# Optimization experiments

Measured on AMD Instinct MI355X. Metric: run time of the kernel, lower is better.

The kernel has to match this reference:

```python
import jax, jax.numpy as jnp
import numpy as np

CW = 64            # channel_width; N = CW**2 = 4096 tokens = d_batch
BIAS = 1.0         # same_channel_bias
D_KQ = 2048
D_V = 2048
STEP = 0           # self.step at first call
T_IDX = 0          # self.t at first call
PE_N = 10000.0


def pe_row(t, d, n=PE_N):
    """Row t of the sinusoidal positional encoding P[t, :] of width d (d even)."""
    i = jnp.arange(d // 2, dtype=jnp.float32)
    denom = jnp.power(jnp.float32(n), 2.0 * i / d)
    ang = jnp.float32(t) / denom
    row = jnp.zeros((d,), dtype=jnp.float32)
    row = row.at[0::2].set(jnp.sin(ang)).at[1::2].set(jnp.cos(ang))
    return row


def setup_inputs() -> dict:
    key = jax.random.key(0)
    ks = jax.random.split(key, 6)
    N = CW * CW          # 4096
    d_in = 2048
    num_steps = 8
    return {
        "x": jax.random.normal(ks[0], (N, d_in), dtype=jnp.float32),
        "W_query": jax.random.uniform(ks[1], (d_in, D_KQ), dtype=jnp.float32),
        "W_key": jax.random.uniform(ks[2], (d_in, D_KQ), dtype=jnp.float32),
        "W_value": jax.random.uniform(ks[3], (d_in, D_V), dtype=jnp.float32),
        "b_channel": jax.random.uniform(ks[4], (N, D_V), dtype=jnp.float32),
        "b_t": jax.random.uniform(ks[5], (num_steps, N, D_V), dtype=jnp.float32),
    }


def reference(x, W_query, W_key, W_value, b_channel, b_t):
    N = x.shape[0]
    q = x @ W_query                      # [N, d_kq]
    k = x @ W_key                        # [N, d_kq]
    v = x @ W_value                      # [N, d_v]
    scores = q @ k.T                     # [N, N]
    # kron(eye(cw), ones(cw,cw)*bias): +bias where tokens share a channel block
    ch = jnp.arange(N) // CW
    scores = scores + jnp.where(ch[:, None] == ch[None, :], jnp.float32(BIAS), jnp.float32(0.0))
    # NOTE: bias added BEFORE the 1/sqrt(d_kq) scaling, as in the original
    attn = jax.nn.softmax(scores / jnp.float32(D_KQ) ** 0.5, axis=-1)
    ctx = attn @ v                       # [N, d_v]
    ctx = ctx + b_channel + b_t[STEP] + pe_row(T_IDX, D_V)
    return ctx
```

## Files before the change

kernel.cpp:

```cpp
#include <hip/hip_runtime.h>
#include <cstdint>
#include <cstddef>


using h8    = __attribute__((ext_vector_type(8))) _Float16;
using h4    = __attribute__((ext_vector_type(4))) _Float16;
using f32x4 = __attribute__((ext_vector_type(4))) float;

__device__ __forceinline__ void gll16(const void* g, void* l) {
  __builtin_amdgcn_global_load_lds(
      (const __attribute__((address_space(1))) uint32_t*)g,
      (__attribute__((address_space(3))) uint32_t*)l, 16, 0, 0);
}

__global__ __launch_bounds__(256) void split_x_kernel(
    const float* __restrict__ X, _Float16* __restrict__ hi,
    _Float16* __restrict__ lo, int n4)
{
  int i = blockIdx.x * 256 + threadIdx.x;
  if (i >= n4) return;
  float4 v = ((const float4*)X)[i];
  float a[4] = {v.x, v.y, v.z, v.w};
  h4 hh, ll;
#pragma unroll
  for (int e = 0; e < 4; ++e) {
    _Float16 h = (_Float16)a[e];
    hh[e] = h;
    ll[e] = (_Float16)(a[e] - (float)h);
  }
  ((h4*)hi)[i] = hh;
  ((h4*)lo)[i] = ll;
}

__global__ __launch_bounds__(256) void transpose_split_w(
    const float* __restrict__ W, _Float16* __restrict__ Thi,
    _Float16* __restrict__ Tlo, int D, int writeLo)
{
  __shared__ float t[32][33];
  int n0 = blockIdx.x * 32;
  int k0 = blockIdx.y * 32;
  int tx = threadIdx.x & 31;
  int ty = threadIdx.x >> 5;
  for (int j = ty; j < 32; j += 8)
    t[j][tx] = W[(size_t)(k0 + j) * D + n0 + tx];
  __syncthreads();
  for (int j = ty; j < 32; j += 8) {
    float v = t[tx][j];
    size_t o = (size_t)(n0 + j) * D + k0 + tx;
    _Float16 h = (_Float16)v;
    Thi[o] = h;
    if (writeLo) Tlo[o] = (_Float16)(v - (float)h);
  }
}

constexpr int EPI_QK = 0;
constexpr int EPI_VT = 1;
constexpr int EPI_S  = 2;
constexpr int EPI_CTX = 3;

template<int EPI, bool SPLIT>
__global__ __launch_bounds__(256, 2) void gemm_bt(
    const _Float16* __restrict__ A, const _Float16* __restrict__ Al,
    const _Float16* __restrict__ B, const _Float16* __restrict__ Bl,
    int K, int lda, int ldb, int ldc, int ldt,
    float* __restrict__ of32, _Float16* __restrict__ oh1,
    _Float16* __restrict__ oh2,
    const float* __restrict__ c1, const float* __restrict__ c2)
{
  __shared__ __align__(16) _Float16 sA [128 * 32];
  __shared__ __align__(16) _Float16 sB [128 * 32];
  __shared__ __align__(16) _Float16 sAl[SPLIT ? 128 * 32 : 8];
  __shared__ __align__(16) _Float16 sBl[SPLIT ? 128 * 32 : 8];

  const int tid  = threadIdx.x;
  const int lane = tid & 63;
  const int wave = tid >> 6;
  const int wm = wave >> 1, wn = wave & 1;
  const int m0 = blockIdx.y * 128, n0 = blockIdx.x * 128;

  const int ca = lane + 64 * wave;
  const int ra = ca >> 2, ka = (ca & 3) * 8;
  const int cc = ca + 256;
  const int rb = cc >> 2, kb = (cc & 3) * 8;
  const size_t lo0 = (size_t)wave * 1024;
  const size_t lo1 = lo0 + 4096;

  const _Float16* gA0 = A + (size_t)(m0 + ra) * lda + ka;
  const _Float16* gA1 = A + (size_t)(m0 + rb) * lda + kb;
  const _Float16* gB0 = B + (size_t)(n0 + ra) * ldb + ka;
  const _Float16* gB1 = B + (size_t)(n0 + rb) * ldb + kb;
  const _Float16* gAl0 = Al ? Al + (size_t)(m0 + ra) * lda + ka : nullptr;
  const _Float16* gAl1 = Al ? Al + (size_t)(m0 + rb) * lda + kb : nullptr;
  const _Float16* gBl0 = Bl ? Bl + (size_t)(n0 + ra) * ldb + ka : nullptr;
  const _Float16* gBl1 = Bl ? Bl + (size_t)(n0 + rb) * ldb + kb : nullptr;

  f32x4 acc[4][4];
#pragma unroll
  for (int i = 0; i < 4; ++i)
#pragma unroll
    for (int j = 0; j < 4; ++j) acc[i][j] = (f32x4){0.f, 0.f, 0.f, 0.f};

  const int fr = lane & 15;
  const int fk = (lane >> 4) * 8;

  for (int k0 = 0; k0 < K; k0 += 32) {
    gll16(gA0 + k0, (char*)sA + lo0);
    gll16(gA1 + k0, (char*)sA + lo1);
    gll16(gB0 + k0, (char*)sB + lo0);
    gll16(gB1 + k0, (char*)sB + lo1);
    if constexpr (SPLIT) {
      gll16(gAl0 + k0, (char*)sAl + lo0);
      gll16(gAl1 + k0, (char*)sAl + lo1);
      gll16(gBl0 + k0, (char*)sBl + lo0);
      gll16(gBl1 + k0, (char*)sBl + lo1);
    }
    __syncthreads();

    h8 af[4], bf[4], afl[4], bfl[4];
#pragma unroll
    for (int mi = 0; mi < 4; ++mi)
      af[mi] = *(const h8*)&sA[(wm * 64 + mi * 16 + fr) * 32 + fk];
#pragma unroll
    for (int ni = 0; ni < 4; ++ni)
      bf[ni] = *(const h8*)&sB[(wn * 64 + ni * 16 + fr) * 32 + fk];
    if constexpr (SPLIT) {
#pragma unroll
      for (int mi = 0; mi < 4; ++mi)
        afl[mi] = *(const h8*)&sAl[(wm * 64 + mi * 16 + fr) * 32 + fk];
#pragma unroll
      for (int ni = 0; ni < 4; ++ni)
        bfl[ni] = *(const h8*)&sBl[(wn * 64 + ni * 16 + fr) * 32 + fk];
    }

#pragma unroll
    for (int mi = 0; mi < 4; ++mi)
#pragma unroll
      for (int ni = 0; ni < 4; ++ni) {
        acc[mi][ni] = __builtin_amdgcn_mfma_f32_16x16x32_f16(
            af[mi], bf[ni], acc[mi][ni], 0, 0, 0);
        if constexpr (SPLIT) {
          acc[mi][ni] = __builtin_amdgcn_mfma_f32_16x16x32_f16(
              af[mi], bfl[ni], acc[mi][ni], 0, 0, 0);
          acc[mi][ni] = __builtin_amdgcn_mfma_f32_16x16x32_f16(
              afl[mi], bf[ni], acc[mi][ni], 0, 0, 0);
        }
      }
    __syncthreads();
  }

  const int drow = (lane >> 4) * 4;
  const int dcol = lane & 15;
#pragma unroll
  for (int mi = 0; mi < 4; ++mi) {
#pragma unroll
    for (int ni = 0; ni < 4; ++ni) {
      const int row = m0 + wm * 64 + mi * 16 + drow;
      const int col = n0 + wn * 64 + ni * 16 + dcol;
      f32x4 v = acc[mi][ni];
      if constexpr (EPI == EPI_S) {
#pragma unroll
        for (int r = 0; r < 4; ++r)
          of32[(size_t)(row + r) * ldc + col] = v[r];
      } else if constexpr (EPI == EPI_QK) {
#pragma unroll
        for (int r = 0; r < 4; ++r) {
          float x = v[r];
          _Float16 hh = (_Float16)x;
          size_t o = (size_t)(row + r) * ldc + col;
          oh1[o] = hh;
          oh2[o] = (_Float16)(x - (float)hh);
        }
      } else if constexpr (EPI == EPI_VT) {
        h4 hh;
#pragma unroll
        for (int r = 0; r < 4; ++r) hh[r] = (_Float16)v[r];
        *(h4*)&oh1[(size_t)col * ldt + row] = hh;
      } else {
#pragma unroll
        for (int r = 0; r < 4; ++r) {
          size_t o = (size_t)(row + r) * ldc + col;
          of32[o] = v[r] + c1[o] + c2[o] + ((col & 1) ? 1.0f : 0.0f);
        }
      }
    }
  }
}

template<int EPI, int NPASS>
__global__ __launch_bounds__(512, 2) void gemm256(
    const _Float16* __restrict__ A0, const _Float16* __restrict__ B0,
    const _Float16* __restrict__ A1, const _Float16* __restrict__ B1,
    const _Float16* __restrict__ A2, const _Float16* __restrict__ B2,
    int lda, int ldb, int ldc,
    float* __restrict__ of32, _Float16* __restrict__ oh1,
    _Float16* __restrict__ oh2)
{
  __shared__ __align__(16) char lds[147456];
  constexpr int T = NPASS * 32;

  const int tid  = threadIdx.x;
  const int lane = tid & 63;
  const int w    = tid >> 6;
  const int wm = w >> 2, wn = w & 3;
  const int fr = lane & 15, sl = lane >> 4;
  const int m0 = blockIdx.y * 256, n0 = blockIdx.x * 256;

  const int sswz  = ((sl ^ ((fr >> 1) & 3)) << 4);
  const int aBase = (wm * 128 + fr) * 64 + sswz;
  const int bBase = 65536 + (wn * 64 + fr) * 64 + sswz;
  const int rowoff = w * 16 + (lane >> 2);
  const int sL8 = ((lane & 3) ^ ((lane >> 3) & 3)) * 8;

  auto gstage = [&](int t, int isB, int kk) {
    const _Float16* g; int ld, r0, gk; char* dst;
    if (t >= T) {
      g = A0; ld = lda; r0 = m0; gk = 0; dst = lds + 131072;
    } else {
      const int p = t >> 5, kt = t & 31;
      g  = isB ? (p == 0 ? B0 : (p == 1 ? B1 : B2))
               : (p == 0 ? A0 : (p == 1 ? A1 : A2));
      ld = isB ? ldb : lda;
      r0 = isB ? n0 : m0;
      gk = kt * 64 + kk * 32;
      dst = lds + (isB ? 65536 : 0) + (t & 1) * 32768 + kk * 16384;
    }
#pragma unroll
    for (int i = 0; i < 2; ++i)
      gll16(g + (size_t)(r0 + i * 128 + rowoff) * ld + gk + sL8,
            dst + i * 8192 + w * 1024);
  };

  f32x4 acc[8][4];
#pragma unroll
  for (int i = 0; i < 8; ++i)
#pragma unroll
    for (int j = 0; j < 4; ++j) acc[i][j] = (f32x4){0.f, 0.f, 0.f, 0.f};

  gstage(0, 0, 0); gstage(0, 1, 0);
  gstage(0, 0, 1); gstage(0, 1, 1);
  gstage(1, 0, 0); gstage(1, 1, 0);
  asm volatile("s_waitcnt vmcnt(8)" ::: "memory");
  __builtin_amdgcn_s_barrier();

#pragma unroll 2
  for (int t = 0; t < T; ++t) {
    const char* aB = lds + (t & 1) * 32768;

#pragma unroll
    for (int kk = 0; kk < 2; ++kk) {
      if (kk == 0) { gstage(t + 1, 0, 1); gstage(t + 1, 1, 1); }
      else         { gstage(t + 2, 0, 0); gstage(t + 2, 1, 0); }

      const char* base = aB + kk * 16384;
      h8 af[8], bf[4];
#pragma unroll
      for (int i = 0; i < 8; ++i)
        af[i] = *(const h8*)(base + aBase + i * 1024);
#pragma unroll
      for (int i = 0; i < 4; ++i)
        bf[i] = *(const h8*)(base + bBase + i * 1024);

      __builtin_amdgcn_s_setprio(1);
#pragma unroll
      for (int mi = 0; mi < 8; ++mi)
#pragma unroll
        for (int ni = 0; ni < 4; ++ni)
          acc[mi][ni] = __builtin_amdgcn_mfma_f32_16x16x32_f16(
              af[mi], bf[ni], acc[mi][ni], 0, 0, 0);
      __builtin_amdgcn_s_setprio(0);

      asm volatile("s_waitcnt vmcnt(8)" ::: "memory");
      __builtin_amdgcn_s_barrier();
    }
  }
  asm volatile("s_waitcnt vmcnt(0)" ::: "memory");

  const int drow = sl * 4;
#pragma unroll
  for (int mi = 0; mi < 8; ++mi) {
#pragma unroll
    for (int ni = 0; ni < 4; ++ni) {
      const int row = m0 + wm * 128 + mi * 16 + drow;
      const int col = n0 + wn * 64 + ni * 16 + fr;
      f32x4 v = acc[mi][ni];
      if constexpr (EPI == EPI_S) {
#pragma unroll
        for (int r = 0; r < 4; ++r)
          of32[(size_t)(row + r) * ldc + col] = v[r];
      } else {
#pragma unroll
        for (int r = 0; r < 4; ++r) {
          float x = v[r];
          _Float16 hh = (_Float16)x;
          size_t o = (size_t)(row + r) * ldc + col;
          oh1[o] = hh;
          oh2[o] = (_Float16)(x - (float)hh);
        }
      }
    }
  }
}

__global__ __launch_bounds__(256) void softmax_bias_kernel(
    float* __restrict__ S, int N)
{
  const float scale = 0.022097086912079608f;
  const int row = blockIdx.x;
  float* rp = S + (size_t)row * N;
  const int cblk = row & ~63;
  const int tid = threadIdx.x;

  float vals[16];
  float mx = -3.0e38f;
#pragma unroll
  for (int it = 0; it < 4; ++it) {
    int base = (it * 256 + tid) * 4;
    float4 v = *(const float4*)(rp + base);
    float a[4] = {v.x, v.y, v.z, v.w};
#pragma unroll
    for (int e = 0; e < 4; ++e) {
      int col = base + e;
      float s = a[e];
      if ((col & ~63) == cblk) s += 1.0f;
      s *= scale;
      vals[it * 4 + e] = s;
      mx = fmaxf(mx, s);
    }
  }
  __shared__ float red[8];
#pragma unroll
  for (int m = 32; m; m >>= 1) mx = fmaxf(mx, __shfl_xor(mx, m, 64));
  if ((tid & 63) == 0) red[tid >> 6] = mx;
  __syncthreads();
  mx = fmaxf(fmaxf(red[0], red[1]), fmaxf(red[2], red[3]));

  float sum = 0.f;
#pragma unroll
  for (int i = 0; i < 16; ++i) {
    float e = __expf(vals[i] - mx);
    vals[i] = e;
    sum += e;
  }
#pragma unroll
  for (int m = 32; m; m >>= 1) sum += __shfl_xor(sum, m, 64);
  if ((tid & 63) == 0) red[4 + (tid >> 6)] = sum;
  __syncthreads();
  sum = red[4] + red[5] + red[6] + red[7];
  float inv = 1.0f / sum;

  _Float16* op = (_Float16*)rp;
#pragma unroll
  for (int it = 0; it < 4; ++it) {
    int base = (it * 256 + tid) * 4;
    h4 hh;
#pragma unroll
    for (int e = 0; e < 4; ++e) hh[e] = (_Float16)(vals[it * 4 + e] * inv);
    *(h4*)(op + base) = hh;
  }
}

extern "C" void kernel_launch(void* const* d_in, const int* in_sizes, int n_in,
                              void* d_out, int out_size, void* d_ws,
                              size_t ws_size, hipStream_t stream)
{
  (void)in_sizes; (void)n_in; (void)out_size; (void)ws_size;
  const float* x   = (const float*)d_in[0];
  const float* Wq  = (const float*)d_in[1];
  const float* Wk  = (const float*)d_in[2];
  const float* Wv  = (const float*)d_in[3];
  const float* bch = (const float*)d_in[4];
  const float* bt0 = (const float*)d_in[5];
  float* out = (float*)d_out;

  char* ws = (char*)d_ws;
  const size_t O_XHI  = 0;
  const size_t O_XLO  = O_XHI + 16777216;
  const size_t O_WQKH = O_XLO + 16777216;
  const size_t O_WQKL = O_WQKH + 16777216;
  const size_t O_S    = 0;
  const size_t O_WVH  = 67108864;
  const size_t O_VT   = O_WVH + 8388608;
  const size_t O_QKH  = O_VT + 16777216;
  const size_t O_QKL  = O_QKH + 33554432;

  _Float16* xhi  = (_Float16*)(ws + O_XHI);
  _Float16* xlo  = (_Float16*)(ws + O_XLO);
  _Float16* wqkh = (_Float16*)(ws + O_WQKH);
  _Float16* wqkl = (_Float16*)(ws + O_WQKL);
  _Float16* wvh  = (_Float16*)(ws + O_WVH);
  _Float16* vT   = (_Float16*)(ws + O_VT);
  _Float16* qkh  = (_Float16*)(ws + O_QKH);
  _Float16* qkl  = (_Float16*)(ws + O_QKL);
  float*    S    = (float*)(ws + O_S);

  split_x_kernel<<<2097152 / 256, 256, 0, stream>>>(x, xhi, xlo, 2097152);
  dim3 tg(64, 64);
  transpose_split_w<<<tg, 256, 0, stream>>>(Wq, wqkh, wqkl, 2048, 1);
  transpose_split_w<<<tg, 256, 0, stream>>>(
      Wk, wqkh + (size_t)2048 * 2048, wqkl + (size_t)2048 * 2048, 2048, 1);
  transpose_split_w<<<tg, 256, 0, stream>>>(Wv, wvh, nullptr, 2048, 0);

  gemm256<EPI_QK, 3><<<dim3(16, 16), 512, 0, stream>>>(
      xhi, wqkh, xhi, wqkl, xlo, wqkh, 2048, 2048, 4096,
      nullptr, qkh, qkl);
  gemm_bt<EPI_VT, false><<<dim3(16, 32), 256, 0, stream>>>(
      xhi, nullptr, wvh, nullptr, 2048, 2048, 2048, 0, 4096,
      nullptr, vT, nullptr, nullptr, nullptr);

  gemm256<EPI_S, 3><<<dim3(16, 16), 512, 0, stream>>>(
      qkh, qkh + 2048, qkh, qkl + 2048, qkl, qkh + 2048, 4096, 4096, 4096,
      S, nullptr, nullptr);

  softmax_bias_kernel<<<4096, 256, 0, stream>>>(S, 4096);

  gemm_bt<EPI_CTX, false><<<dim3(16, 32), 256, 0, stream>>>(
      (const _Float16*)S, nullptr, vT, nullptr, 4096, 8192, 4096, 2048, 0,
      out, nullptr, nullptr, bch, bt0);
}
```

Before: 932.5 us.

## Use triple-buffered LDS ring with register double-buffered fragments in GEMM

Restructures the main GEMM loop from a 2-slot, split-k staging scheme into a 3-slot ring of 32-wide k substeps, with A and B fragments double-buffered in registers. The next substep's LDS reads are issued before the current MFMA block so LDS latency overlaps matrix math, and LDS use drops. In exchange it doubles fragment registers, which could pressure the 2-waves-per-SIMD launch bound. It also relies on a single barrier per substep to guard ring-slot reuse.

```diff
diff --git a/kernel.cpp b/kernel.cpp
--- a/kernel.cpp
+++ b/kernel.cpp
@@ -195,8 +195,8 @@
     float* __restrict__ of32, _Float16* __restrict__ oh1,
     _Float16* __restrict__ oh2)
 {
-  __shared__ __align__(16) char lds[147456];
-  constexpr int T = NPASS * 32;
+  __shared__ __align__(16) char lds[114688];
+  constexpr int S = NPASS * 64;
 
   const int tid  = threadIdx.x;
   const int lane = tid & 63;
@@ -207,27 +207,31 @@
 
   const int sswz  = ((sl ^ ((fr >> 1) & 3)) << 4);
   const int aBase = (wm * 128 + fr) * 64 + sswz;
-  const int bBase = 65536 + (wn * 64 + fr) * 64 + sswz;
+  const int bBase = 16384 + (wn * 64 + fr) * 64 + sswz;
   const int rowoff = w * 16 + (lane >> 2);
   const int sL8 = ((lane & 3) ^ ((lane >> 3) & 3)) * 8;
 
-  auto gstage = [&](int t, int isB, int kk) {
-    const _Float16* g; int ld, r0, gk; char* dst;
-    if (t >= T) {
-      g = A0; ld = lda; r0 = m0; gk = 0; dst = lds + 131072;
+  auto gstage = [&](int u) {
+    const _Float16 *gA, *gB; int gk; char *dstA, *dstB;
+    if (u >= S) {
+      gA = A0; gB = B0; gk = 0;
+      dstA = lds + 98304; dstB = lds + 98304;
     } else {
-      const int p = t >> 5, kt = t & 31;
-      g  = isB ? (p == 0 ? B0 : (p == 1 ? B1 : B2))
-               : (p == 0 ? A0 : (p == 1 ? A1 : A2));
-      ld = isB ? ldb : lda;
-      r0 = isB ? n0 : m0;
-      gk = kt * 64 + kk * 32;
-      dst = lds + (isB ? 65536 : 0) + (t & 1) * 32768 + kk * 16384;
+      const int p = u >> 6, ku = u & 63;
+      gA = (p == 0 ? A0 : (p == 1 ? A1 : A2));
+      gB = (p == 0 ? B0 : (p == 1 ? B1 : B2));
+      gk = ku * 32;
+      char* base = lds + (u % 3) * 32768;
+      dstA = base; dstB = base + 16384;
     }
 #pragma unroll
     for (int i = 0; i < 2; ++i)
-      gll16(g + (size_t)(r0 + i * 128 + rowoff) * ld + gk + sL8,
-            dst + i * 8192 + w * 1024);
+      gll16(gA + (size_t)(m0 + i * 128 + rowoff) * lda + gk + sL8,
+            dstA + i * 8192 + w * 1024);
+#pragma unroll
+    for (int i = 0; i < 2; ++i)
+      gll16(gB + (size_t)(n0 + i * 128 + rowoff) * ldb + gk + sL8,
+            dstB + i * 8192 + w * 1024);
   };
 
   f32x4 acc[8][4];
@@ -236,42 +240,55 @@
 #pragma unroll
     for (int j = 0; j < 4; ++j) acc[i][j] = (f32x4){0.f, 0.f, 0.f, 0.f};
 
-  gstage(0, 0, 0); gstage(0, 1, 0);
-  gstage(0, 0, 1); gstage(0, 1, 1);
-  gstage(1, 0, 0); gstage(1, 1, 0);
-  asm volatile("s_waitcnt vmcnt(8)" ::: "memory");
+  h8 af0[8], bf0[4], af1[8], bf1[4];
+
+  auto ldset0 = [&](int u) {
+    const char* ub = lds + (u % 3) * 32768;
+#pragma unroll
+    for (int i = 0; i < 8; ++i) af0[i] = *(const h8*)(ub + aBase + i * 1024);
+#pragma unroll
+    for (int i = 0; i < 4; ++i) bf0[i] = *(const h8*)(ub + bBase + i * 1024);
+  };
+  auto ldset1 = [&](int u) {
+    const char* ub = lds + (u % 3) * 32768;
+#pragma unroll
+    for (int i = 0; i < 8; ++i) af1[i] = *(const h8*)(ub + aBase + i * 1024);
+#pragma unroll
+    for (int i = 0; i < 4; ++i) bf1[i] = *(const h8*)(ub + bBase + i * 1024);
+  };
+
+  gstage(0); gstage(1); gstage(2);
+  asm volatile("s_waitcnt vmcnt(4)" ::: "memory");
   __builtin_amdgcn_s_barrier();
-
-#pragma unroll 2
-  for (int t = 0; t < T; ++t) {
-    const char* aB = lds + (t & 1) * 32768;
-
-#pragma unroll
-    for (int kk = 0; kk < 2; ++kk) {
-      if (kk == 0) { gstage(t + 1, 0, 1); gstage(t + 1, 1, 1); }
-      else         { gstage(t + 2, 0, 0); gstage(t + 2, 1, 0); }
-
-      const char* base = aB + kk * 16384;
-      h8 af[8], bf[4];
-#pragma unroll
-      for (int i = 0; i < 8; ++i)
-        af[i] = *(const h8*)(base + aBase + i * 1024);
-#pragma unroll
-      for (int i = 0; i < 4; ++i)
-        bf[i] = *(const h8*)(base + bBase + i * 1024);
-
-      __builtin_amdgcn_s_setprio(1);
-#pragma unroll
-      for (int mi = 0; mi < 8; ++mi)
-#pragma unroll
-        for (int ni = 0; ni < 4; ++ni)
-          acc[mi][ni] = __builtin_amdgcn_mfma_f32_16x16x32_f16(
-              af[mi], bf[ni], acc[mi][ni], 0, 0, 0);
-      __builtin_amdgcn_s_setprio(0);
-
-      asm volatile("s_waitcnt vmcnt(8)" ::: "memory");
-      __builtin_amdgcn_s_barrier();
-    }
+  ldset0(0);
+
+#pragma unroll 1
+  for (int s = 0; s < S; s += 2) {
+    gstage(s + 3);
+    ldset1(s + 1);
+    __builtin_amdgcn_s_setprio(1);
+#pragma unroll
+    for (int mi = 0; mi < 8; ++mi)
+#pragma unroll
+      for (int ni = 0; ni < 4; ++ni)
+        acc[mi][ni] = __builtin_amdgcn_mfma_f32_16x16x32_f16(
+            af0[mi], bf0[ni], acc[mi][ni], 0, 0, 0);
+    __builtin_amdgcn_s_setprio(0);
+    asm volatile("s_waitcnt vmcnt(4)" ::: "memory");
+    __builtin_amdgcn_s_barrier();
+
+    gstage(s + 4);
+    ldset0(s + 2);
+    __builtin_amdgcn_s_setprio(1);
+#pragma unroll
+    for (int mi = 0; mi < 8; ++mi)
+#pragma unroll
+      for (int ni = 0; ni < 4; ++ni)
+        acc[mi][ni] = __builtin_amdgcn_mfma_f32_16x16x32_f16(
+            af1[mi], bf1[ni], acc[mi][ni], 0, 0, 0);
+    __builtin_amdgcn_s_setprio(0);
+    asm volatile("s_waitcnt vmcnt(4)" ::: "memory");
+    __builtin_amdgcn_s_barrier();
   }
   asm volatile("s_waitcnt vmcnt(0)" ::: "memory");
 
```

New measurement: 2.125 ms. 128% more time.
